# Kernel optimization log

Measured on AMD Instinct MI355X. Metric: run time of the kernel, lower is better.

## Reference

```python
import jax, jax.numpy as jnp
import numpy as np

N = 50000   # nodes per graph stream
E = 800000  # edges per graph stream
G = 100     # graphs in batch
FIN, H = 74, 256


def setup_inputs() -> dict:
    key = jax.random.key(0)
    ks = jax.random.split(key, 16)
    d = {
        'xl': jax.random.normal(ks[0], (N, FIN), jnp.float32),
        'xr': jax.random.normal(ks[1], (N, FIN), jnp.float32),
        'src_l': jax.random.randint(ks[2], (E,), 0, N, jnp.int32),
        'dst_l': jax.random.randint(ks[3], (E,), 0, N, jnp.int32),
        'src_r': jax.random.randint(ks[4], (E,), 0, N, jnp.int32),
        'dst_r': jax.random.randint(ks[5], (E,), 0, N, jnp.int32),
        'gid_l': jnp.sort(jax.random.randint(ks[6], (N,), 0, G, jnp.int32)),
        'gid_r': jnp.sort(jax.random.randint(ks[7], (N,), 0, G, jnp.int32)),
        'W0': jax.random.normal(ks[8], (FIN, H), jnp.float32) / np.sqrt(FIN),
        'b0': jnp.zeros((H,), jnp.float32),
        'W1': jax.random.normal(ks[9], (H, H), jnp.float32) / np.sqrt(H),
        'b1': jnp.zeros((H,), jnp.float32),
        'W2': jax.random.normal(ks[10], (H, H), jnp.float32) / np.sqrt(H),
        'b2': jnp.zeros((H,), jnp.float32),
        'Wf1': jax.random.normal(ks[11], (2 * H, H), jnp.float32) / np.sqrt(2 * H),
        'bf1': jnp.zeros((H,), jnp.float32),
        'Wf2': jax.random.normal(ks[12], (H, 1), jnp.float32) / np.sqrt(H),
        'bf2': jnp.zeros((1,), jnp.float32),
    }
    return d


def _deg_isqrt(idx, n):
    deg = jax.ops.segment_sum(jnp.ones_like(idx, jnp.float32), idx, num_segments=n)
    return jax.lax.rsqrt(jnp.maximum(deg, 1.0))


def _graph_conv(x, src, dst, do_isq, di_isq, W, b):
    # DGL GraphConv, norm='both': h = relu(D_in^{-1/2} A D_out^{-1/2} X W + b)
    h = (x * do_isq[:, None]) @ W            # transform-first (in_feats >= out for layer0 path is fine mathematically)
    agg = jax.ops.segment_sum(h[src], dst, num_segments=x.shape[0])
    return jax.nn.relu(agg * di_isq[:, None] + b)


def reference(xl, xr, src_l, dst_l, src_r, dst_r, gid_l, gid_r,
              W0, b0, W1, b1, W2, b2, Wf1, bf1, Wf2, bf2):
    do_l, di_l = _deg_isqrt(src_l, N), _deg_isqrt(dst_l, N)
    do_r, di_r = _deg_isqrt(src_r, N), _deg_isqrt(dst_r, N)
    Ws, bs = (W0, W1, W2), (b0, b1, b2)
    hl, hr = xl, xr
    for W, b in zip(Ws, bs):  # shared weights across both graph streams
        hl = _graph_conv(hl, src_l, dst_l, do_l, di_l, W, b)
        hr = _graph_conv(hr, src_r, dst_r, do_r, di_r, W, b)
    pl = jax.ops.segment_sum(hl, gid_l, num_segments=G)  # dgl.sum_nodes
    pr = jax.ops.segment_sum(hr, gid_r, num_segments=G)
    z = jnp.concatenate([pl, pr], axis=-1)               # [G, 2H]
    return jax.nn.relu(z @ Wf1 + bf1) @ Wf2 + bf2        # [G, 1]
```

## Files before the change

kernel.cpp:

```cpp
#include <hip/hip_runtime.h>

#define N_NODES 50000
#define N_EDGES 800000
#define N_GRAPHS 100
#define FIN_DIM 74
#define K0 96
#define H_DIM 256
#define EG 3125
#define XS2_BLKS 9375
#define WCONV_BLKS 608
#define AGG0_BLKS 3128
#define AGGH_BLKS 6256
#define GEMM_BLKS 782
#define POOL_BLKS 782
#define SCAN_BLOCKS 196

typedef float f32x4 __attribute__((ext_vector_type(4)));
typedef float f32x2 __attribute__((ext_vector_type(2)));
typedef unsigned int u32x4 __attribute__((ext_vector_type(4)));
typedef unsigned short us2 __attribute__((ext_vector_type(2)));
typedef unsigned short us8 __attribute__((ext_vector_type(8)));
typedef __bf16 bf16x8 __attribute__((ext_vector_type(8)));

__device__ __forceinline__ unsigned short f2bf(float x) {
    unsigned u = __builtin_bit_cast(unsigned, x);
    u += 0x7fff + ((u >> 16) & 1);
    return (unsigned short)(u >> 16);
}
__device__ __forceinline__ float bf2f(unsigned short h) {
    return __builtin_bit_cast(float, (unsigned)h << 16);
}
__device__ __forceinline__ void acc8(float* a, us8 v) {
    u32x4 w = __builtin_bit_cast(u32x4, v);
    #pragma unroll
    for (int i = 0; i < 4; ++i) {
        a[2 * i]     += __builtin_bit_cast(float, w[i] << 16);
        a[2 * i + 1] += __builtin_bit_cast(float, w[i] & 0xffff0000u);
    }
}


__device__ __forceinline__ void hist_body(int bid, const int* __restrict__ src,
                                          const int* __restrict__ dst,
                                          int* __restrict__ cs, int* __restrict__ fc,
                                          int* __restrict__ rk) {
    int e = bid * 256 + threadIdx.x;
    if (e < N_EDGES) {
        rk[e] = atomicAdd(&fc[dst[e]], 1);
        atomicAdd(&cs[src[e]], 1);
    }
}

__device__ __forceinline__ void scat_body(int bid, const int* __restrict__ src,
                                          const int* __restrict__ dst,
                                          const int* __restrict__ rp,
                                          const int* __restrict__ rk,
                                          int* __restrict__ col) {
    int e = bid * 256 + threadIdx.x;
    if (e < N_EDGES) {
        int d = dst[e];
        col[rp[d] + rk[e]] = src[e];
    }
}

__device__ __forceinline__ void xscale_body(int bid, const float* __restrict__ x,
                                            const float* __restrict__ dso,
                                            unsigned short* __restrict__ xp) {
    int id = bid * 256 + threadIdx.x;
    int n = id / 48, f = (id - n * 48) * 2;
    float v0 = 0.f, v1 = 0.f;
    if (f < FIN_DIM) {
        f32x2 t = *(const f32x2*)&x[(size_t)n * FIN_DIM + f];
        float d = dso[n];
        v0 = t[0] * d; v1 = t[1] * d;
    }
    us2 r = { f2bf(v0), f2bf(v1) };
    *(us2*)&xp[(size_t)(f >> 4) * (N_NODES * 16) + (size_t)n * 16 + (f & 15)] = r;
}

__device__ __forceinline__ void wconv_body(int bid, const float* __restrict__ W0,
                                           const float* __restrict__ W1,
                                           const float* __restrict__ W2,
                                           unsigned short* __restrict__ Wt) {
    int id = bid * 256 + threadIdx.x;
    if (id < 256 * 96) {
        int n = id / 96, k = id - n * 96;
        float v = (k < FIN_DIM) ? W0[(size_t)k * H_DIM + n] : 0.f;
        Wt[id] = f2bf(v);
    } else if (id < 256 * 96 + 65536) {
        int id2 = id - 256 * 96;
        int n = id2 >> 8, k = id2 & 255;
        Wt[id] = f2bf(W1[(size_t)k * H_DIM + n]);
    } else {
        int id3 = id - 256 * 96 - 65536;
        int n = id3 >> 8, k = id3 & 255;
        Wt[id] = f2bf(W2[(size_t)k * H_DIM + n]);
    }
}

template<int SW, int NACT, int NSL>
__device__ __forceinline__ void agg_body(int abid, int cg,
                                         const unsigned short* __restrict__ h,
                                         const int* __restrict__ rp,
                                         const int* __restrict__ col,
                                         unsigned short* __restrict__ A) {
    const int CPB = SW / 8;
    const int NPB = 256 / CPB;
    if (cg >= NSL) return;
    int slot = threadIdx.x & (CPB - 1);
    int n = (abid >> 3) * NPB + threadIdx.x / CPB;
    if (n >= N_NODES) return;
    unsigned short* dst = A + (size_t)cg * (N_NODES * SW) + (size_t)n * SW + slot * 8;
    if (cg >= NACT) { us8 z = {}; *(us8*)dst = z; return; }
    const unsigned short* hs = h + (size_t)cg * (N_NODES * SW) + slot * 8;
    int beg = rp[n], end = rp[n + 1];
    float a[8] = {};
    int j = beg;
    for (; j + 3 < end; j += 4) {
        int s0 = col[j], s1 = col[j + 1], s2 = col[j + 2], s3 = col[j + 3];
        us8 v0 = *(const us8*)(hs + (size_t)s0 * SW);
        us8 v1 = *(const us8*)(hs + (size_t)s1 * SW);
        us8 v2 = *(const us8*)(hs + (size_t)s2 * SW);
        us8 v3 = *(const us8*)(hs + (size_t)s3 * SW);
        acc8(a, v0); acc8(a, v1); acc8(a, v2); acc8(a, v3);
    }
    for (; j < end; ++j)
        acc8(a, *(const us8*)(hs + (size_t)col[j] * SW));
    us8 r;
    #pragma unroll
    for (int i = 0; i < 8; ++i) r[i] = f2bf(a[i]);
    *(us8*)dst = r;
}

__device__ __forceinline__ void pool_body(int nb, const unsigned short* __restrict__ h,
                                          const int* __restrict__ gid,
                                          float* __restrict__ pool) {
    int n0 = nb * 64;
    int f = threadIdx.x;
    const unsigned short* hf = h + (size_t)(f >> 5) * (N_NODES * 32) + (f & 31);
    int end = min(n0 + 64, N_NODES);
    float acc = 0.0f;
    int gcur = gid[n0];
    for (int i = n0; i < end; ++i) {
        int g = gid[i];
        if (g != gcur) {
            atomicAdd(&pool[(size_t)gcur * H_DIM + f], acc);
            acc = 0.0f;
            gcur = g;
        }
        acc += bf2f(hf[(size_t)i * 32]);
    }
    atomicAdd(&pool[(size_t)gcur * H_DIM + f], acc);
}

template<int K, int SW>
__device__ __forceinline__ void gemm_body(int id, const unsigned short* __restrict__ A,
                                          const unsigned short* __restrict__ Wt,
                                          const float* __restrict__ bias,
                                          const float* __restrict__ dsi,
                                          const float* __restrict__ scale,
                                          unsigned short* __restrict__ C,
                                          unsigned short* smem) {
    unsigned short (*Ah)[40] = (unsigned short(*)[40])smem;
    unsigned short (*Bh)[40] = (unsigned short(*)[40])(smem + 128 * 40);
    const int M = N_NODES;

    int tid = threadIdx.x;
    int lane = tid & 63, wid = tid >> 6;
    int wm = (wid >> 1) * 64, wn = (wid & 1) * 64;
    int bm = (id >> 1) * 128, bn = (id & 1) * 128;

    f32x4 acc[4][4] = {};
    int r0 = wm + (lane & 15);
    int c0 = wn + (lane & 15);
    int kA = (lane >> 4) * 8;

    for (int k0 = 0; k0 < K; k0 += 32) {
        #pragma unroll
        for (int i = 0; i < 2; ++i) {
            int q = tid + i * 256;
            int row = q >> 2, k8 = (q & 3) * 8;
            int gm = bm + row;
            int kk = k0 + k8;
            us8 v = {};
            if (gm < M)
                v = *(const us8*)(A + (size_t)(kk / SW) * ((size_t)N_NODES * SW)
                                    + (size_t)gm * SW + (kk % SW));
            *(us8*)&Ah[row][k8] = v;
        }
        {
            int colx = tid & 127, kg = tid >> 7;
            const unsigned short* wsrc = Wt + (size_t)(bn + colx) * K + k0 + kg * 16;
            us8 w0 = *(const us8*)(wsrc);
            us8 w1 = *(const us8*)(wsrc + 8);
            *(us8*)&Bh[colx][kg * 16] = w0;
            *(us8*)&Bh[colx][kg * 16 + 8] = w1;
        }
        __syncthreads();

        bf16x8 ah[4], bh[4];
        #pragma unroll
        for (int m = 0; m < 4; ++m)
            ah[m] = __builtin_bit_cast(bf16x8, *(const us8*)&Ah[r0 + m * 16][kA]);
        #pragma unroll
        for (int n = 0; n < 4; ++n)
            bh[n] = __builtin_bit_cast(bf16x8, *(const us8*)&Bh[c0 + n * 16][kA]);

        #pragma unroll
        for (int m = 0; m < 4; ++m)
            #pragma unroll
            for (int n = 0; n < 4; ++n)
                acc[m][n] = __builtin_amdgcn_mfma_f32_16x16x32_bf16(ah[m], bh[n], acc[m][n], 0, 0, 0);
        __syncthreads();
    }

    int rowq = (lane >> 4) * 4;
    #pragma unroll
    for (int n = 0; n < 4; ++n) {
        int gn = bn + wn + n * 16 + (lane & 15);
        float bv = bias[gn];
        unsigned short* cs = C + (size_t)(gn >> 5) * (N_NODES * 32) + (gn & 31);
        #pragma unroll
        for (int m = 0; m < 4; ++m) {
            #pragma unroll
            for (int j = 0; j < 4; ++j) {
                int gm = bm + wm + m * 16 + rowq + j;
                if (gm < M) {
                    float r = fmaxf(acc[m][n][j] * dsi[gm] + bv, 0.0f);
                    if (scale) r *= scale[gm];
                    cs[(size_t)gm * 32] = f2bf(r);
                }
            }
        }
    }
}


__device__ __forceinline__ int block_excl_scan(int v, int* wsums) {
    int lane = threadIdx.x & 63, w = threadIdx.x >> 6;
    int x = v;
    #pragma unroll
    for (int ofs = 1; ofs < 64; ofs <<= 1) {
        int y = __shfl_up(x, ofs, 64);
        if (lane >= ofs) x += y;
    }
    if (lane == 63) wsums[w] = x;
    __syncthreads();
    int wo = 0;
    #pragma unroll
    for (int k = 0; k < 4; ++k) if (k < w) wo += wsums[k];
    return wo + x - v;
}

__global__ void k_hist2(const float* __restrict__ W0, const float* __restrict__ W1,
                        const float* __restrict__ W2, unsigned short* __restrict__ Wt,
                        const int* __restrict__ srcL, const int* __restrict__ dstL,
                        int* __restrict__ csL, int* __restrict__ fcL, int* __restrict__ rkL,
                        const int* __restrict__ srcR, const int* __restrict__ dstR,
                        int* __restrict__ csR, int* __restrict__ fcR, int* __restrict__ rkR) {
    int bid = blockIdx.x;
    if (bid < WCONV_BLKS)           wconv_body(bid, W0, W1, W2, Wt);
    else if (bid < WCONV_BLKS + EG) hist_body(bid - WCONV_BLKS, srcL, dstL, csL, fcL, rkL);
    else                            hist_body(bid - WCONV_BLKS - EG, srcR, dstR, csR, fcR, rkR);
}

__global__ void deg_scan1_kernel(const int* __restrict__ csL, const int* __restrict__ fcL,
                                 float* __restrict__ dsoL, float* __restrict__ dsiL,
                                 int* __restrict__ rpL, int* __restrict__ bsL,
                                 const int* __restrict__ csR, const int* __restrict__ fcR,
                                 float* __restrict__ dsoR, float* __restrict__ dsiR,
                                 int* __restrict__ rpR, int* __restrict__ bsR) {
    const int* cs = blockIdx.y ? csR : csL;
    const int* fc = blockIdx.y ? fcR : fcL;
    float* dso = blockIdx.y ? dsoR : dsoL;
    float* dsi = blockIdx.y ? dsiR : dsiL;
    int* rp = blockIdx.y ? rpR : rpL;
    int* bs = blockIdx.y ? bsR : bsL;
    __shared__ int ws[4];
    int i = blockIdx.x * 256 + threadIdx.x;
    int v = 0;
    if (i < N_NODES) {
        dso[i] = rsqrtf(fmaxf((float)cs[i], 1.0f));
        v = fc[i];
        dsi[i] = rsqrtf(fmaxf((float)v, 1.0f));
    }
    int ex = block_excl_scan(v, ws);
    if (i < N_NODES) rp[i] = ex;
    if (threadIdx.x == 255) bs[blockIdx.x] = ex + v;
}

__global__ void scan23_kernel(int* __restrict__ rpL, const int* __restrict__ bsL,
                              int* __restrict__ rpR, const int* __restrict__ bsR) {
    int* rp = blockIdx.y ? rpR : rpL;
    const int* bs = blockIdx.y ? bsR : bsL;
    __shared__ int ws[4];
    __shared__ int s_off;
    int b = blockIdx.x;
    int v = (threadIdx.x < b && threadIdx.x < SCAN_BLOCKS) ? bs[threadIdx.x] : 0;
    int ex = block_excl_scan(v, ws);
    if (threadIdx.x == 255) s_off = ex + v;
    __syncthreads();
    int i = b * 256 + threadIdx.x;
    if (i < N_NODES) rp[i] += s_off;
    if (i == 0) rp[N_NODES] = N_EDGES;
}

__global__ void fuse_ssxx(const int* __restrict__ srcL, const int* __restrict__ dstL,
                          const int* __restrict__ rpL, const int* __restrict__ rkL,
                          int* __restrict__ colL,
                          const int* __restrict__ srcR, const int* __restrict__ dstR,
                          const int* __restrict__ rpR, const int* __restrict__ rkR,
                          int* __restrict__ colR,
                          const float* __restrict__ xL, const float* __restrict__ dsoL,
                          unsigned short* __restrict__ xpL,
                          const float* __restrict__ xR, const float* __restrict__ dsoR,
                          unsigned short* __restrict__ xpR) {
    int bid = blockIdx.x;
    if (bid < EG)                         scat_body(bid, srcL, dstL, rpL, rkL, colL);
    else if (bid < 2 * EG)                scat_body(bid - EG, srcR, dstR, rpR, rkR, colR);
    else if (bid < 2 * EG + XS2_BLKS)     xscale_body(bid - 2 * EG, xL, dsoL, xpL);
    else                                  xscale_body(bid - 2 * EG - XS2_BLKS, xR, dsoR, xpR);
}

__global__ void fuse_agg2_l0(const unsigned short* __restrict__ hL, const int* __restrict__ rpL,
                             const int* __restrict__ colL, unsigned short* __restrict__ AL,
                             const unsigned short* __restrict__ hR, const int* __restrict__ rpR,
                             const int* __restrict__ colR, unsigned short* __restrict__ AR) {
    int bid = blockIdx.x;
    if (bid < AGG0_BLKS) agg_body<16, 5, 6>(bid, bid & 7, hL, rpL, colL, AL);
    else {
        int lb = bid - AGG0_BLKS;
        agg_body<16, 5, 6>(lb, lb & 7, hR, rpR, colR, AR);
    }
}

__global__ void fuse_agg2_h(const unsigned short* __restrict__ hL, const int* __restrict__ rpL,
                            const int* __restrict__ colL, unsigned short* __restrict__ AL,
                            const unsigned short* __restrict__ hR, const int* __restrict__ rpR,
                            const int* __restrict__ colR, unsigned short* __restrict__ AR) {
    int bid = blockIdx.x;
    if (bid < AGGH_BLKS) agg_body<32, 8, 8>(bid, bid & 7, hL, rpL, colL, AL);
    else {
        int lb = bid - AGGH_BLKS;
        agg_body<32, 8, 8>(lb, lb & 7, hR, rpR, colR, AR);
    }
}

template<int K, int SW>
__global__ __launch_bounds__(256) void gemm_pair2(
        const unsigned short* __restrict__ AL, const float* __restrict__ dsiL,
        const float* __restrict__ scL, unsigned short* __restrict__ CL,
        const unsigned short* __restrict__ AR, const float* __restrict__ dsiR,
        const float* __restrict__ scR, unsigned short* __restrict__ CR,
        const unsigned short* __restrict__ Wt, const float* __restrict__ bias) {
    __shared__ unsigned short smem[2 * 128 * 40];
    int bid = blockIdx.x;
    if (bid < GEMM_BLKS) gemm_body<K, SW>(bid, AL, Wt, bias, dsiL, scL, CL, smem);
    else                 gemm_body<K, SW>(bid - GEMM_BLKS, AR, Wt, bias, dsiR, scR, CR, smem);
}

__global__ void pool2_kernel(const unsigned short* __restrict__ hL, const int* __restrict__ gidL,
                             float* __restrict__ poolL,
                             const unsigned short* __restrict__ hR, const int* __restrict__ gidR,
                             float* __restrict__ poolR) {
    int bid = blockIdx.x;
    if (bid < POOL_BLKS) pool_body(bid, hL, gidL, poolL);
    else                 pool_body(bid - POOL_BLKS, hR, gidR, poolR);
}

__global__ __launch_bounds__(256) void mlp_kernel(
        const float* __restrict__ pl, const float* __restrict__ pr,
        const float* __restrict__ Wf1, const float* __restrict__ bf1,
        const float* __restrict__ Wf2, const float* __restrict__ bf2,
        float* __restrict__ out) {
    __shared__ float z[512];
    __shared__ float red[256];
    int g = blockIdx.x, tid = threadIdx.x;
    z[tid] = pl[(size_t)g * H_DIM + tid];
    z[tid + 256] = pr[(size_t)g * H_DIM + tid];
    __syncthreads();
    float t = bf1[tid];
    #pragma unroll 8
    for (int k = 0; k < 512; ++k) t += z[k] * Wf1[(size_t)k * H_DIM + tid];
    t = fmaxf(t, 0.0f);
    red[tid] = t * Wf2[tid];
    __syncthreads();
    for (int ofs = 128; ofs > 0; ofs >>= 1) {
        if (tid < ofs) red[tid] += red[tid + ofs];
        __syncthreads();
    }
    if (tid == 0) out[g] = red[0] + bf2[0];
}


extern "C" void kernel_launch(void* const* d_in, const int* in_sizes, int n_in,
                              void* d_out, int out_size, void* d_ws, size_t ws_size,
                              hipStream_t stream) {
    const float* xl   = (const float*)d_in[0];
    const float* xr   = (const float*)d_in[1];
    const int* src_l  = (const int*)d_in[2];
    const int* dst_l  = (const int*)d_in[3];
    const int* src_r  = (const int*)d_in[4];
    const int* dst_r  = (const int*)d_in[5];
    const int* gid_l  = (const int*)d_in[6];
    const int* gid_r  = (const int*)d_in[7];
    const float* W0   = (const float*)d_in[8];
    const float* b0   = (const float*)d_in[9];
    const float* W1   = (const float*)d_in[10];
    const float* b1   = (const float*)d_in[11];
    const float* W2   = (const float*)d_in[12];
    const float* b2   = (const float*)d_in[13];
    const float* Wf1  = (const float*)d_in[14];
    const float* bf1  = (const float*)d_in[15];
    const float* Wf2  = (const float*)d_in[16];
    const float* bf2  = (const float*)d_in[17];
    float* out = (float*)d_out;
    (void)in_sizes; (void)n_in; (void)out_size; (void)ws_size;

    size_t off = 0;
    auto carve = [&](size_t bytes) {
        void* p = (char*)d_ws + off;
        off += (bytes + 255) & ~(size_t)255;
        return p;
    };
    const size_t NB4 = (size_t)N_NODES * 4;

    char* zstart = (char*)d_ws;
    int*   cs_l   = (int*)carve(NB4);
    int*   fc_l   = (int*)carve(NB4);
    int*   cs_r   = (int*)carve(NB4);
    int*   fc_r   = (int*)carve(NB4);
    float* pool_l = (float*)carve((size_t)N_GRAPHS * H_DIM * 4);
    float* pool_r = (float*)carve((size_t)N_GRAPHS * H_DIM * 4);
    size_t zbytes = off;

    float* dso_l = (float*)carve(NB4);
    float* dsi_l = (float*)carve(NB4);
    float* dso_r = (float*)carve(NB4);
    float* dsi_r = (float*)carve(NB4);
    int*   rp_l  = (int*)carve((size_t)(N_NODES + 1) * 4);
    int*   rp_r  = (int*)carve((size_t)(N_NODES + 1) * 4);
    int*   col_l = (int*)carve((size_t)N_EDGES * 4);
    int*   col_r = (int*)carve((size_t)N_EDGES * 4);
    int*   rk_l  = (int*)carve((size_t)N_EDGES * 4);
    int*   rk_r  = (int*)carve((size_t)N_EDGES * 4);
    int*   bs_l  = (int*)carve((size_t)SCAN_BLOCKS * 4);
    int*   bs_r  = (int*)carve((size_t)SCAN_BLOCKS * 4);

    unsigned short* Wt    = (unsigned short*)carve((size_t)(256 * 96 + 2 * 65536) * 2);
    unsigned short* Wt0   = Wt;
    unsigned short* Wt1   = Wt + 256 * 96;
    unsigned short* Wt2   = Wt + 256 * 96 + 65536;
    unsigned short* xp_l  = (unsigned short*)carve((size_t)N_NODES * 96 * 2);
    unsigned short* xp_r  = (unsigned short*)carve((size_t)N_NODES * 96 * 2);
    unsigned short* bufA_l = (unsigned short*)carve((size_t)N_NODES * H_DIM * 2);
    unsigned short* bufA_r = (unsigned short*)carve((size_t)N_NODES * H_DIM * 2);
    unsigned short* bufH_l = (unsigned short*)carve((size_t)N_NODES * H_DIM * 2);
    unsigned short* bufH_r = (unsigned short*)carve((size_t)N_NODES * H_DIM * 2);

    hipMemsetAsync(zstart, 0, zbytes, stream);

    k_hist2<<<WCONV_BLKS + 2 * EG, 256, 0, stream>>>(
        W0, W1, W2, Wt,
        src_l, dst_l, cs_l, fc_l, rk_l,
        src_r, dst_r, cs_r, fc_r, rk_r);

    deg_scan1_kernel<<<dim3(SCAN_BLOCKS, 2), 256, 0, stream>>>(
        cs_l, fc_l, dso_l, dsi_l, rp_l, bs_l,
        cs_r, fc_r, dso_r, dsi_r, rp_r, bs_r);
    scan23_kernel<<<dim3(SCAN_BLOCKS, 2), 256, 0, stream>>>(rp_l, bs_l, rp_r, bs_r);

    fuse_ssxx<<<2 * EG + 2 * XS2_BLKS, 256, 0, stream>>>(
        src_l, dst_l, rp_l, rk_l, col_l,
        src_r, dst_r, rp_r, rk_r, col_r,
        xl, dso_l, xp_l,
        xr, dso_r, xp_r);

    fuse_agg2_l0<<<2 * AGG0_BLKS, 256, 0, stream>>>(
        xp_l, rp_l, col_l, bufA_l,
        xp_r, rp_r, col_r, bufA_r);
    gemm_pair2<K0, 16><<<2 * GEMM_BLKS, 256, 0, stream>>>(
        bufA_l, dsi_l, dso_l, bufH_l,
        bufA_r, dsi_r, dso_r, bufH_r,
        Wt0, b0);

    fuse_agg2_h<<<2 * AGGH_BLKS, 256, 0, stream>>>(
        bufH_l, rp_l, col_l, bufA_l,
        bufH_r, rp_r, col_r, bufA_r);
    gemm_pair2<H_DIM, 32><<<2 * GEMM_BLKS, 256, 0, stream>>>(
        bufA_l, dsi_l, dso_l, bufH_l,
        bufA_r, dsi_r, dso_r, bufH_r,
        Wt1, b1);

    fuse_agg2_h<<<2 * AGGH_BLKS, 256, 0, stream>>>(
        bufH_l, rp_l, col_l, bufA_l,
        bufH_r, rp_r, col_r, bufA_r);
    gemm_pair2<H_DIM, 32><<<2 * GEMM_BLKS, 256, 0, stream>>>(
        bufA_l, dsi_l, nullptr, bufH_l,
        bufA_r, dsi_r, nullptr, bufH_r,
        Wt2, b2);

    pool2_kernel<<<2 * POOL_BLKS, 256, 0, stream>>>(
        bufH_l, gid_l, pool_l,
        bufH_r, gid_r, pool_r);
    mlp_kernel<<<N_GRAPHS, 256, 0, stream>>>(pool_l, pool_r, Wf1, bf1, Wf2, bf2, out);
}
```

Baseline: 738.1 us.

## Fuse graph sum-pooling into final GEMM epilogue via shared-memory atomics

The last GraphConv GEMM now does the per-graph sum pooling in its epilogue instead of writing the layer-3 activations to global memory and running a separate pool kernel. Each block accumulates relu outputs into a shared-memory buffer indexed by graph offset from the block's first graph, and falls back to global atomics beyond GSPAN graphs. The buffer is then flushed to the global pool with atomics. This removes a full bf16 activation write/read and one kernel launch, at the cost of LDS atomic contention and extra global atomics. Pooling now sums fp32 values rather than bf16-rounded ones.

After: 814.8 us. 1.1x slower.

```diff
diff --git a/kernel.cpp b/kernel.cpp
--- a/kernel.cpp
+++ b/kernel.cpp
@@ -12,8 +12,8 @@
 #define AGG0_BLKS 3128
 #define AGGH_BLKS 6256
 #define GEMM_BLKS 782
-#define POOL_BLKS 782
 #define SCAN_BLOCKS 196
+#define GSPAN 16
 
 typedef float f32x4 __attribute__((ext_vector_type(4)));
 typedef float f32x2 __attribute__((ext_vector_type(2)));
@@ -132,34 +132,15 @@
     *(us8*)dst = r;
 }
 
-__device__ __forceinline__ void pool_body(int nb, const unsigned short* __restrict__ h,
-                                          const int* __restrict__ gid,
-                                          float* __restrict__ pool) {
-    int n0 = nb * 64;
-    int f = threadIdx.x;
-    const unsigned short* hf = h + (size_t)(f >> 5) * (N_NODES * 32) + (f & 31);
-    int end = min(n0 + 64, N_NODES);
-    float acc = 0.0f;
-    int gcur = gid[n0];
-    for (int i = n0; i < end; ++i) {
-        int g = gid[i];
-        if (g != gcur) {
-            atomicAdd(&pool[(size_t)gcur * H_DIM + f], acc);
-            acc = 0.0f;
-            gcur = g;
-        }
-        acc += bf2f(hf[(size_t)i * 32]);
-    }
-    atomicAdd(&pool[(size_t)gcur * H_DIM + f], acc);
-}
-
-template<int K, int SW>
+template<int K, int SW, bool POOL>
 __device__ __forceinline__ void gemm_body(int id, const unsigned short* __restrict__ A,
                                           const unsigned short* __restrict__ Wt,
                                           const float* __restrict__ bias,
                                           const float* __restrict__ dsi,
                                           const float* __restrict__ scale,
                                           unsigned short* __restrict__ C,
+                                          const int* __restrict__ gid,
+                                          float* __restrict__ pool,
                                           unsigned short* smem) {
     unsigned short (*Ah)[40] = (unsigned short(*)[40])smem;
     unsigned short (*Bh)[40] = (unsigned short(*)[40])(smem + 128 * 40);
@@ -215,22 +196,55 @@
     }
 
     int rowq = (lane >> 4) * 4;
-    #pragma unroll
-    for (int n = 0; n < 4; ++n) {
-        int gn = bn + wn + n * 16 + (lane & 15);
-        float bv = bias[gn];
-        unsigned short* cs = C + (size_t)(gn >> 5) * (N_NODES * 32) + (gn & 31);
+    if constexpr (!POOL) {
         #pragma unroll
-        for (int m = 0; m < 4; ++m) {
+        for (int n = 0; n < 4; ++n) {
+            int gn = bn + wn + n * 16 + (lane & 15);
+            float bv = bias[gn];
+            unsigned short* cs = C + (size_t)(gn >> 5) * (N_NODES * 32) + (gn & 31);
             #pragma unroll
-            for (int j = 0; j < 4; ++j) {
-                int gm = bm + wm + m * 16 + rowq + j;
-                if (gm < M) {
-                    float r = fmaxf(acc[m][n][j] * dsi[gm] + bv, 0.0f);
-                    if (scale) r *= scale[gm];
-                    cs[(size_t)gm * 32] = f2bf(r);
+            for (int m = 0; m < 4; ++m) {
+                #pragma unroll
+                for (int j = 0; j < 4; ++j) {
+                    int gm = bm + wm + m * 16 + rowq + j;
+                    if (gm < M) {
+                        float r = fmaxf(acc[m][n][j] * dsi[gm] + bv, 0.0f);
+                        if (scale) r *= scale[gm];
+                        cs[(size_t)gm * 32] = f2bf(r);
+                    }
                 }
             }
+        }
+    } else {
+        float* pbuf = (float*)smem;
+        for (int i = tid; i < GSPAN * 128; i += 256) pbuf[i] = 0.f;
+        __syncthreads();
+        int gid0 = gid[bm];
+        #pragma unroll
+        for (int n = 0; n < 4; ++n) {
+            int lcol = wn + n * 16 + (lane & 15);
+            float bv = bias[bn + lcol];
+            #pragma unroll
+            for (int m = 0; m < 4; ++m) {
+                #pragma unroll
+                for (int j = 0; j < 4; ++j) {
+                    int gm = bm + wm + m * 16 + rowq + j;
+                    if (gm < M) {
+                        float r = fmaxf(acc[m][n][j] * dsi[gm] + bv, 0.0f);
+                        int g = gid[gm] - gid0;
+                        if (g < GSPAN) atomicAdd(&pbuf[g * 128 + lcol], r);
+                        else atomicAdd(&pool[(size_t)gid[gm] * H_DIM + bn + lcol], r);
+                    }
+                }
+            }
+        }
+        __syncthreads();
+        for (int i = tid; i < GSPAN * 128; i += 256) {
+            float v = pbuf[i];
+            int gs = i >> 7, lc = i & 127;
+            int gg = gid0 + gs;
+            if (v != 0.f && gg < N_GRAPHS)
+                atomicAdd(&pool[(size_t)gg * H_DIM + bn + lc], v);
         }
     }
 }
@@ -346,26 +360,21 @@
     }
 }
 
-template<int K, int SW>
+template<int K, int SW, bool POOL>
 __global__ __launch_bounds__(256) void gemm_pair2(
         const unsigned short* __restrict__ AL, const float* __restrict__ dsiL,
         const float* __restrict__ scL, unsigned short* __restrict__ CL,
+        const int* __restrict__ gidL, float* __restrict__ poolL,
         const unsigned short* __restrict__ AR, const float* __restrict__ dsiR,
         const float* __restrict__ scR, unsigned short* __restrict__ CR,
+        const int* __restrict__ gidR, float* __restrict__ poolR,
         const unsigned short* __restrict__ Wt, const float* __restrict__ bias) {
     __shared__ unsigned short smem[2 * 128 * 40];
     int bid = blockIdx.x;
-    if (bid < GEMM_BLKS) gemm_body<K, SW>(bid, AL, Wt, bias, dsiL, scL, CL, smem);
-    else                 gemm_body<K, SW>(bid - GEMM_BLKS, AR, Wt, bias, dsiR, scR, CR, smem);
-}
-
-__global__ void pool2_kernel(const unsigned short* __restrict__ hL, const int* __restrict__ gidL,
-                             float* __restrict__ poolL,
-                             const unsigned short* __restrict__ hR, const int* __restrict__ gidR,
-                             float* __restrict__ poolR) {
-    int bid = blockIdx.x;
-    if (bid < POOL_BLKS) pool_body(bid, hL, gidL, poolL);
-    else                 pool_body(bid - POOL_BLKS, hR, gidR, poolR);
+    if (bid < GEMM_BLKS)
+        gemm_body<K, SW, POOL>(bid, AL, Wt, bias, dsiL, scL, CL, gidL, poolL, smem);
+    else
+        gemm_body<K, SW, POOL>(bid - GEMM_BLKS, AR, Wt, bias, dsiR, scR, CR, gidR, poolR, smem);
 }
 
 __global__ __launch_bounds__(256) void mlp_kernel(
@@ -479,29 +488,26 @@
     fuse_agg2_l0<<<2 * AGG0_BLKS, 256, 0, stream>>>(
         xp_l, rp_l, col_l, bufA_l,
         xp_r, rp_r, col_r, bufA_r);
-    gemm_pair2<K0, 16><<<2 * GEMM_BLKS, 256, 0, stream>>>(
-        bufA_l, dsi_l, dso_l, bufH_l,
-        bufA_r, dsi_r, dso_r, bufH_r,
+    gemm_pair2<K0, 16, false><<<2 * GEMM_BLKS, 256, 0, stream>>>(
+        bufA_l, dsi_l, dso_l, bufH_l, nullptr, nullptr,
+        bufA_r, dsi_r, dso_r, bufH_r, nullptr, nullptr,
         Wt0, b0);
 
     fuse_agg2_h<<<2 * AGGH_BLKS, 256, 0, stream>>>(
         bufH_l, rp_l, col_l, bufA_l,
         bufH_r, rp_r, col_r, bufA_r);
-    gemm_pair2<H_DIM, 32><<<2 * GEMM_BLKS, 256, 0, stream>>>(
-        bufA_l, dsi_l, dso_l, bufH_l,
-        bufA_r, dsi_r, dso_r, bufH_r,
+    gemm_pair2<H_DIM, 32, false><<<2 * GEMM_BLKS, 256, 0, stream>>>(
+        bufA_l, dsi_l, dso_l, bufH_l, nullptr, nullptr,
+        bufA_r, dsi_r, dso_r, bufH_r, nullptr, nullptr,
         Wt1, b1);
 
     fuse_agg2_h<<<2 * AGGH_BLKS, 256, 0, stream>>>(
         bufH_l, rp_l, col_l, bufA_l,
         bufH_r, rp_r, col_r, bufA_r);
-    gemm_pair2<H_DIM, 32><<<2 * GEMM_BLKS, 256, 0, stream>>>(
-        bufA_l, dsi_l, nullptr, bufH_l,
-        bufA_r, dsi_r, nullptr, bufH_r,
+    gemm_pair2<H_DIM, 32, true><<<2 * GEMM_BLKS, 256, 0, stream>>>(
+        bufA_l, dsi_l, nullptr, nullptr, gid_l, pool_l,
+        bufA_r, dsi_r, nullptr, nullptr, gid_r, pool_r,
         Wt2, b2);
 
-    pool2_kernel<<<2 * POOL_BLKS, 256, 0, stream>>>(
-        bufH_l, gid_l, pool_l,
-        bufH_r, gid_r, pool_r);
     mlp_kernel<<<N_GRAPHS, 256, 0, stream>>>(pool_l, pool_r, Wf1, bf1, Wf2, bf2, out);
 }
```
